# Kernel optimization log

Measured on AMD Instinct MI355X. Metric: run time of the kernel, lower is better.

Reference implementation:

```python
import jax, jax.numpy as jnp
import numpy as np

B, S, D = 2, 2048, 1024
H, DH = 16, 64  # num_heads, hidden_dimension (per-head)


def setup_inputs() -> dict:
    key = jax.random.key(0)
    ks = jax.random.split(key, 9)
    s = 1.0 / np.sqrt(D)
    so = 1.0 / np.sqrt(H * DH)
    return {
        "x": jax.random.normal(ks[0], (B, S, D), dtype=jnp.float32),
        "Wq": jax.random.uniform(ks[1], (D, H * DH), jnp.float32, -s, s),
        "bq": jax.random.uniform(ks[2], (H * DH,), jnp.float32, -s, s),
        "Wk": jax.random.uniform(ks[3], (D, H * DH), jnp.float32, -s, s),
        "bk": jax.random.uniform(ks[4], (H * DH,), jnp.float32, -s, s),
        "Wv": jax.random.uniform(ks[5], (D, H * DH), jnp.float32, -s, s),
        "bv": jax.random.uniform(ks[6], (H * DH,), jnp.float32, -s, s),
        "Wo": jax.random.uniform(ks[7], (H * DH, D), jnp.float32, -so, so),
        "bo": jax.random.uniform(ks[8], (D,), jnp.float32, -so, so),
    }


def reference(x, Wq, bq, Wk, bk, Wv, bv, Wo, bo):
    b, s, _ = x.shape
    # project and split heads: [b, h, s, dh]
    q = (x @ Wq + bq).reshape(b, s, H, DH).transpose(0, 2, 1, 3)
    k = (x @ Wk + bk).reshape(b, s, H, DH).transpose(0, 2, 1, 3)
    v = (x @ Wv + bv).reshape(b, s, H, DH).transpose(0, 2, 1, 3)
    scores = jnp.einsum('bhqd,bhkd->bhqk', q, k) / jnp.sqrt(jnp.float32(DH))
    causal = jnp.triu(jnp.ones((s, s), dtype=bool), k=1)
    scores = jnp.where(causal, -jnp.inf, scores)
    weights = jax.nn.softmax(scores, axis=-1)
    out = jnp.einsum('bhqk,bhkd->bhqd', weights, v)
    out = out.transpose(0, 2, 1, 3).reshape(b, s, H * DH)
    return out @ Wo + bo
```

## Files before the change

kernel.cpp:

```cpp
#include <hip/hip_runtime.h>

#define B_  2
#define S_  2048
#define D_  1024
#define H_  16
#define DH_ 64
#define NDH (H_*DH_)
#define BS_ (B_*S_)
#define PER ((size_t)B_*H_*S_*DH_)

typedef __bf16 bf16;
typedef bf16 bf16x8 __attribute__((ext_vector_type(8)));
typedef bf16 bf16x4 __attribute__((ext_vector_type(4)));
typedef float f32x4 __attribute__((ext_vector_type(4)));

#define QSCALE 0.18033688011112042f

#define AS1 __attribute__((address_space(1)))
#define AS3 __attribute__((address_space(3)))
__device__ inline void gld16(const bf16* g, bf16* l) {
    __builtin_amdgcn_global_load_lds((const AS1 void*)g, (AS3 void*)l, 16, 0, 0);
}

__global__ __launch_bounds__(256) void prep(
        const float* __restrict__ x,
        const float* __restrict__ W0, const float* __restrict__ W1,
        const float* __restrict__ W2, const float* __restrict__ W3,
        bf16* __restrict__ xb, bf16* __restrict__ T0, bf16* __restrict__ T1,
        bf16* __restrict__ T2, bf16* __restrict__ T3) {
    __shared__ float T[32][33];
    int bid = blockIdx.x, t = threadIdx.x;
    if (bid < 4096) {
        int i = (bid * 256 + t) * 4;
        float4 v = *(const float4*)(x + i);
        bf16x4 o = { (bf16)v.x, (bf16)v.y, (bf16)v.z, (bf16)v.w };
        *(bf16x4*)(xb + i) = o;
        return;
    }
    int r2 = bid - 4096;
    int z = r2 >> 10, w = r2 & 1023;
    const float* W = (z == 0) ? W0 : (z == 1) ? W1 : (z == 2) ? W2 : W3;
    bf16* Wt = (z == 0) ? T0 : (z == 1) ? T1 : (z == 2) ? T2 : T3;
    int k0 = (w >> 5) * 32, n0 = (w & 31) * 32;
    int r = t >> 3, c = (t & 7) * 4;
    float4 v = *(const float4*)(W + (size_t)(k0 + r) * 1024 + n0 + c);
    T[c + 0][r] = v.x; T[c + 1][r] = v.y; T[c + 2][r] = v.z; T[c + 3][r] = v.w;
    __syncthreads();
    bf16x4 o = { (bf16)T[r][c], (bf16)T[r][c + 1], (bf16)T[r][c + 2], (bf16)T[r][c + 3] };
    *(bf16x4*)(Wt + (size_t)(n0 + r) * 1024 + k0 + c) = o;
}

__global__ __launch_bounds__(256) void qkv_gemm(
        const bf16* __restrict__ A, const bf16* __restrict__ Bt,
        const float* __restrict__ bq, const float* __restrict__ bk,
        const float* __restrict__ bv, bf16* __restrict__ Qout, bf16* __restrict__ Vt) {
    __shared__ __align__(16) bf16 As[2][128 * 32];
    __shared__ __align__(16) bf16 Bs[2][128 * 32];
    int tid = threadIdx.x, wave = tid >> 6, lane = tid & 63;
    int quad = lane >> 4, l16 = lane & 15;

    int flat = blockIdx.y * 24 + blockIdx.x;
    int swz  = (flat & 7) * 96 + (flat >> 3);
    int bm = (swz / 24) * 128, bn = (swz % 24) * 128;
    int wm = (wave >> 1) * 64, wn = (wave & 1) * 64;

    int sr = lane >> 2, sc = (lane & 3) * 8;
    const bf16* Ag0 = A + (size_t)(bm + (wave * 2 + 0) * 16 + sr) * 1024 + sc;
    const bf16* Ag1 = A + (size_t)(bm + (wave * 2 + 1) * 16 + sr) * 1024 + sc;
    const bf16* Bg0 = Bt + (size_t)(bn + (wave * 2 + 0) * 16 + sr) * 1024 + sc;
    const bf16* Bg1 = Bt + (size_t)(bn + (wave * 2 + 1) * 16 + sr) * 1024 + sc;
    int la0 = (wave * 2 + 0) * 512;
    int la1 = (wave * 2 + 1) * 512;

    f32x4 acc[4][4] = {};

    gld16(Ag0, &As[0][la0]);
    gld16(Ag1, &As[0][la1]);
    gld16(Bg0, &Bs[0][la0]);
    gld16(Bg1, &Bs[0][la1]);
    asm volatile("s_waitcnt vmcnt(0)" ::: "memory");
    __builtin_amdgcn_s_barrier();

    for (int t = 0; t < 32; ++t) {
        int cur = t & 1, nxt = cur ^ 1;
        if (t < 31) {
            int k0 = (t + 1) * 32;
            gld16(Ag0 + k0, &As[nxt][la0]);
            gld16(Ag1 + k0, &As[nxt][la1]);
            gld16(Bg0 + k0, &Bs[nxt][la0]);
            gld16(Bg1 + k0, &Bs[nxt][la1]);
        }
        bf16x8 af[4], bfr[4];
        #pragma unroll
        for (int i = 0; i < 4; ++i)
            af[i] = *(const bf16x8*)&As[cur][(wm + i * 16 + l16) * 32 + quad * 8];
        #pragma unroll
        for (int j = 0; j < 4; ++j)
            bfr[j] = *(const bf16x8*)&Bs[cur][(wn + j * 16 + l16) * 32 + quad * 8];
        #pragma unroll
        for (int i = 0; i < 4; ++i)
          #pragma unroll
          for (int j = 0; j < 4; ++j)
            acc[i][j] = __builtin_amdgcn_mfma_f32_16x16x32_bf16(af[i], bfr[j], acc[i][j], 0, 0, 0);
        asm volatile("s_waitcnt vmcnt(0)" ::: "memory");
        __builtin_amdgcn_s_barrier();
    }

    #pragma unroll
    for (int i = 0; i < 4; ++i)
      #pragma unroll
      for (int j = 0; j < 4; ++j) {
        int col = bn + wn + j * 16 + l16;
        float bias = (col < 1024) ? bq[col] : (col < 2048) ? bk[col - 1024] : bv[col - 2048];
        int qkv = col >> 10, cw = col & 1023;
        int hh = cw >> 6, d = cw & 63;
        int row0 = bm + wm + i * 16 + quad * 4;
        int bb = row0 >> 11, s0 = row0 & 2047;
        if (qkv < 2) {
            float scl = (qkv == 0) ? QSCALE : 1.0f;
            #pragma unroll
            for (int r = 0; r < 4; ++r)
                Qout[(size_t)qkv * PER + (((size_t)bb * H_ + hh) * S_ + s0 + r) * DH_ + d] =
                    (bf16)((acc[i][j][r] + bias) * scl);
        } else {
            bf16x4 pack;
            #pragma unroll
            for (int r = 0; r < 4; ++r) pack[r] = (bf16)(acc[i][j][r] + bias);
            *(bf16x4*)&Vt[(((size_t)bb * H_ + hh) * DH_ + d) * S_ + s0] = pack;
        }
      }
}

__global__ __launch_bounds__(256) void gemm_proj(
        const bf16* __restrict__ A, const bf16* __restrict__ Bt,
        const float* __restrict__ bias, float* __restrict__ out) {
    __shared__ __align__(16) bf16 As[2][128 * 32];
    __shared__ __align__(16) bf16 Bs[2][64 * 32];
    int tid = threadIdx.x, wave = tid >> 6, lane = tid & 63;
    int quad = lane >> 4, l16 = lane & 15;

    int flat = blockIdx.y * 16 + blockIdx.x;
    int swz  = (flat & 7) * 64 + (flat >> 3);
    int bm = (swz / 16) * 128, bn = (swz % 16) * 64;
    int wm = (wave >> 1) * 64, wn = (wave & 1) * 32;

    int sr = lane >> 2, sc = (lane & 3) * 8;
    const bf16* Ag0 = A + (size_t)(bm + (wave * 2 + 0) * 16 + sr) * 1024 + sc;
    const bf16* Ag1 = A + (size_t)(bm + (wave * 2 + 1) * 16 + sr) * 1024 + sc;
    const bf16* Bg0 = Bt + (size_t)(bn + wave * 16 + sr) * 1024 + sc;
    int la0 = (wave * 2 + 0) * 512;
    int la1 = (wave * 2 + 1) * 512;
    int lb0 = wave * 512;

    f32x4 acc[4][2] = {};

    gld16(Ag0, &As[0][la0]);
    gld16(Ag1, &As[0][la1]);
    gld16(Bg0, &Bs[0][lb0]);
    asm volatile("s_waitcnt vmcnt(0)" ::: "memory");
    __builtin_amdgcn_s_barrier();

    for (int t = 0; t < 32; ++t) {
        int cur = t & 1, nxt = cur ^ 1;
        if (t < 31) {
            int k0 = (t + 1) * 32;
            gld16(Ag0 + k0, &As[nxt][la0]);
            gld16(Ag1 + k0, &As[nxt][la1]);
            gld16(Bg0 + k0, &Bs[nxt][lb0]);
        }
        bf16x8 af[4], bfr[2];
        #pragma unroll
        for (int i = 0; i < 4; ++i)
            af[i] = *(const bf16x8*)&As[cur][(wm + i * 16 + l16) * 32 + quad * 8];
        #pragma unroll
        for (int j = 0; j < 2; ++j)
            bfr[j] = *(const bf16x8*)&Bs[cur][(wn + j * 16 + l16) * 32 + quad * 8];
        #pragma unroll
        for (int i = 0; i < 4; ++i)
          #pragma unroll
          for (int j = 0; j < 2; ++j)
            acc[i][j] = __builtin_amdgcn_mfma_f32_16x16x32_bf16(af[i], bfr[j], acc[i][j], 0, 0, 0);
        asm volatile("s_waitcnt vmcnt(0)" ::: "memory");
        __builtin_amdgcn_s_barrier();
    }

    #pragma unroll
    for (int i = 0; i < 4; ++i)
      #pragma unroll
      for (int j = 0; j < 2; ++j) {
        int col = bn + wn + j * 16 + l16;
        float b = bias[col];
        #pragma unroll
        for (int r = 0; r < 4; ++r) {
            int row = bm + wm + i * 16 + quad * 4 + r;
            out[(size_t)row * 1024 + col] = acc[i][j][r] + b;
        }
      }
}

__global__ __launch_bounds__(256) void flash10(
        const bf16* __restrict__ Q, const bf16* __restrict__ K,
        const bf16* __restrict__ Vt, bf16* __restrict__ O) {
    int bh = blockIdx.x;
    int b = bh >> 4, h = bh & 15;
    int t = 31 - blockIdx.y;
    int q0 = t * 64;
    int nkt = t + 1;
    int tid = threadIdx.x;
    int wave = tid >> 6, lane = tid & 63;
    int quad = lane >> 4, l16 = lane & 15;
    int lm = l16 & 7;

    __shared__ __align__(16) bf16 Kl[2][64 * 64];
    __shared__ __align__(16) bf16 Vl[2][64 * 64];
    __shared__ bf16 P[4][16][72];

    const bf16* Qb = Q + (size_t)bh * S_ * DH_;
    const bf16* Kb = K + (size_t)bh * S_ * DH_;
    const bf16* Vb = Vt + (size_t)bh * DH_ * S_;

    bf16x8 qf[2];
    {
        const bf16* qp = Qb + (size_t)(q0 + wave * 16 + l16) * DH_ + quad * 8;
        qf[0] = *(const bf16x8*)(qp);
        qf[1] = *(const bf16x8*)(qp + 32);
    }

    bf16x8 ones;
    #pragma unroll
    for (int j = 0; j < 8; ++j) ones[j] = (l16 == 0) ? (bf16)1.0f : (bf16)0.0f;

    f32x4 oacc[4] = {};
    f32x4 lacc = {};

    int r8 = lane >> 3, c8 = lane & 7;
    int sco = ((c8 ^ r8) * 8);

    auto stage = [&](int buf, int kt) {
        int kv0 = kt * 64;
        #pragma unroll
        for (int g = 0; g < 2; ++g) {
            int row = wave * 16 + g * 8;
            gld16(Kb + (size_t)(kv0 + row + r8) * DH_ + sco, &Kl[buf][row * 64]);
            gld16(Vb + (size_t)(row + r8) * S_ + kv0 + sco,   &Vl[buf][row * 64]);
        }
    };

    stage(0, 0);
    __syncthreads();

    for (int kt = 0; kt < nkt; ++kt) {
        int buf = kt & 1;
        if (kt + 1 < nkt) stage(buf ^ 1, kt + 1);
        int kv0 = kt * 64;

        bf16x8 kf[4][2];
        #pragma unroll
        for (int ns = 0; ns < 4; ++ns) {
            int row = ns * 16 + l16;
            kf[ns][0] = *(const bf16x8*)&Kl[buf][row * 64 + ((quad)     ^ lm) * 8];
            kf[ns][1] = *(const bf16x8*)&Kl[buf][row * 64 + ((4 + quad) ^ lm) * 8];
        }

        f32x4 sacc[4] = {};
        #pragma unroll
        for (int ns = 0; ns < 4; ++ns) {
            sacc[ns] = __builtin_amdgcn_mfma_f32_16x16x32_bf16(qf[0], kf[ns][0], sacc[ns], 0, 0, 0);
            sacc[ns] = __builtin_amdgcn_mfma_f32_16x16x32_bf16(qf[1], kf[ns][1], sacc[ns], 0, 0, 0);
        }

        bool diag = (kt == nkt - 1);
        #pragma unroll
        for (int ns = 0; ns < 4; ++ns)
          #pragma unroll
          for (int r = 0; r < 4; ++r) {
              float p = __builtin_amdgcn_exp2f(sacc[ns][r]);
              if (diag) {
                  int kv = kv0 + ns * 16 + l16;
                  int qq = q0 + wave * 16 + quad * 4 + r;
                  if (kv > qq) p = 0.f;
              }
              P[wave][quad * 4 + r][ns * 16 + l16] = (bf16)p;
          }

        #pragma unroll
        for (int ks = 0; ks < 2; ++ks) {
            bf16x8 pf = *(const bf16x8*)&P[wave][l16][ks * 32 + quad * 8];
            lacc = __builtin_amdgcn_mfma_f32_16x16x32_bf16(pf, ones, lacc, 0, 0, 0);
            #pragma unroll
            for (int ds = 0; ds < 4; ++ds) {
                bf16x8 vf = *(const bf16x8*)&Vl[buf][(ds * 16 + l16) * 64 + ((ks * 4 + quad) ^ lm) * 8];
                oacc[ds] = __builtin_amdgcn_mfma_f32_16x16x32_bf16(pf, vf, oacc[ds], 0, 0, 0);
            }
        }

        __syncthreads();
    }

    float ls[4];
    #pragma unroll
    for (int r = 0; r < 4; ++r) ls[r] = __shfl(lacc[r], quad << 4);
    #pragma unroll
    for (int ds = 0; ds < 4; ++ds)
      #pragma unroll
      for (int r = 0; r < 4; ++r) {
          int qq = q0 + wave * 16 + quad * 4 + r;
          O[((size_t)b * S_ + qq) * NDH + h * DH_ + ds * 16 + l16] = (bf16)(oacc[ds][r] / ls[r]);
      }
}

extern "C" void kernel_launch(void* const* d_in, const int* in_sizes, int n_in,
                              void* d_out, int out_size, void* d_ws, size_t ws_size,
                              hipStream_t stream) {
    const float* x  = (const float*)d_in[0];
    const float* Wq = (const float*)d_in[1];
    const float* bq = (const float*)d_in[2];
    const float* Wk = (const float*)d_in[3];
    const float* bk = (const float*)d_in[4];
    const float* Wv = (const float*)d_in[5];
    const float* bv = (const float*)d_in[6];
    const float* Wo = (const float*)d_in[7];
    const float* bo = (const float*)d_in[8];
    float* out = (float*)d_out;

    bf16* ws = (bf16*)d_ws;
    const size_t M1 = (size_t)1024 * 1024;
    bf16* xb    = ws;
    bf16* WqkvT = ws + 4 * M1;
    bf16* WoT   = ws + 7 * M1;
    bf16* Qw    = ws + 8 * M1;
    bf16* Vtw   = ws + 16 * M1;
    bf16* Ow    = ws + 20 * M1;

    prep<<<8192, 256, 0, stream>>>(x, Wq, Wk, Wv, Wo,
                                   xb, WqkvT, WqkvT + M1, WqkvT + 2 * M1, WoT);

    qkv_gemm<<<dim3(3072 / 128, BS_ / 128), 256, 0, stream>>>(xb, WqkvT, bq, bk, bv, Qw, Vtw);

    flash10<<<dim3(B_ * H_, 32), 256, 0, stream>>>(Qw, Qw + PER, Vtw, Ow);

    gemm_proj<<<dim3(1024 / 64, BS_ / 128), 256, 0, stream>>>(Ow, WoT, bo, out);
}
```

Measured before the change: 189.2 us.

## Triple-buffer GEMM K-loop and XOR-swizzle LDS tiles to cut bank conflicts

Both the QKV and output-projection GEMMs move from a double-buffered to a triple-buffered LDS pipeline. Loads run two k-tiles ahead, a partial vmcnt wait lets one stage stay in flight, and there is one barrier per iteration instead of a full drain. The global-to-LDS column chunk is XOR-swizzled by row, and the fragment reads apply the matching swizzle, to reduce LDS bank conflicts on the 16-byte row reads. This costs 50% more shared memory per block, which may lower occupancy, and relies on hand-counted vmcnt values being correct.

```diff
diff --git a/kernel.cpp b/kernel.cpp
--- a/kernel.cpp
+++ b/kernel.cpp
@@ -54,8 +54,8 @@
         const bf16* __restrict__ A, const bf16* __restrict__ Bt,
         const float* __restrict__ bq, const float* __restrict__ bk,
         const float* __restrict__ bv, bf16* __restrict__ Qout, bf16* __restrict__ Vt) {
-    __shared__ __align__(16) bf16 As[2][128 * 32];
-    __shared__ __align__(16) bf16 Bs[2][128 * 32];
+    __shared__ __align__(16) bf16 As[3][128 * 32];
+    __shared__ __align__(16) bf16 Bs[3][128 * 32];
     int tid = threadIdx.x, wave = tid >> 6, lane = tid & 63;
     int quad = lane >> 4, l16 = lane & 15;
 
@@ -64,7 +64,8 @@
     int bm = (swz / 24) * 128, bn = (swz % 24) * 128;
     int wm = (wave >> 1) * 64, wn = (wave & 1) * 64;
 
-    int sr = lane >> 2, sc = (lane & 3) * 8;
+    int sr = lane >> 2;
+    int sc = (((lane & 3) ^ ((sr ^ (sr >> 2)) & 3)) * 8);
     const bf16* Ag0 = A + (size_t)(bm + (wave * 2 + 0) * 16 + sr) * 1024 + sc;
     const bf16* Ag1 = A + (size_t)(bm + (wave * 2 + 1) * 16 + sr) * 1024 + sc;
     const bf16* Bg0 = Bt + (size_t)(bn + (wave * 2 + 0) * 16 + sr) * 1024 + sc;
@@ -72,39 +73,43 @@
     int la0 = (wave * 2 + 0) * 512;
     int la1 = (wave * 2 + 1) * 512;
 
+    int cs0 = ((0 ^ ((l16 ^ (l16 >> 2)) & 3)) ^ quad) * 8;
+    int rsw = (l16 ^ (l16 >> 2)) & 3;
+
     f32x4 acc[4][4] = {};
 
-    gld16(Ag0, &As[0][la0]);
-    gld16(Ag1, &As[0][la1]);
-    gld16(Bg0, &Bs[0][la0]);
-    gld16(Bg1, &Bs[0][la1]);
-    asm volatile("s_waitcnt vmcnt(0)" ::: "memory");
-    __builtin_amdgcn_s_barrier();
+    auto stage = [&](int buf, int t) {
+        int k0 = t * 32;
+        gld16(Ag0 + k0, &As[buf][la0]);
+        gld16(Ag1 + k0, &As[buf][la1]);
+        gld16(Bg0 + k0, &Bs[buf][la0]);
+        gld16(Bg1 + k0, &Bs[buf][la1]);
+    };
+    (void)cs0;
+
+    stage(0, 0);
+    stage(1, 1);
 
     for (int t = 0; t < 32; ++t) {
-        int cur = t & 1, nxt = cur ^ 1;
-        if (t < 31) {
-            int k0 = (t + 1) * 32;
-            gld16(Ag0 + k0, &As[nxt][la0]);
-            gld16(Ag1 + k0, &As[nxt][la1]);
-            gld16(Bg0 + k0, &Bs[nxt][la0]);
-            gld16(Bg1 + k0, &Bs[nxt][la1]);
-        }
+        if (t < 30) asm volatile("s_waitcnt vmcnt(4)" ::: "memory");
+        else        asm volatile("s_waitcnt vmcnt(0)" ::: "memory");
+        __builtin_amdgcn_s_barrier();
+        if (t + 2 < 32) stage((t + 2) % 3, t + 2);
+        int cur = t % 3;
         bf16x8 af[4], bfr[4];
         #pragma unroll
         for (int i = 0; i < 4; ++i)
-            af[i] = *(const bf16x8*)&As[cur][(wm + i * 16 + l16) * 32 + quad * 8];
+            af[i] = *(const bf16x8*)&As[cur][(wm + i * 16 + l16) * 32 + ((0 ^ quad ^ rsw)) * 8];
         #pragma unroll
         for (int j = 0; j < 4; ++j)
-            bfr[j] = *(const bf16x8*)&Bs[cur][(wn + j * 16 + l16) * 32 + quad * 8];
+            bfr[j] = *(const bf16x8*)&Bs[cur][(wn + j * 16 + l16) * 32 + ((0 ^ quad ^ rsw)) * 8];
         #pragma unroll
         for (int i = 0; i < 4; ++i)
           #pragma unroll
           for (int j = 0; j < 4; ++j)
             acc[i][j] = __builtin_amdgcn_mfma_f32_16x16x32_bf16(af[i], bfr[j], acc[i][j], 0, 0, 0);
-        asm volatile("s_waitcnt vmcnt(0)" ::: "memory");
-        __builtin_amdgcn_s_barrier();
-    }
+    }
+    __builtin_amdgcn_s_barrier();
 
     #pragma unroll
     for (int i = 0; i < 4; ++i)
@@ -134,8 +139,8 @@
 __global__ __launch_bounds__(256) void gemm_proj(
         const bf16* __restrict__ A, const bf16* __restrict__ Bt,
         const float* __restrict__ bias, float* __restrict__ out) {
-    __shared__ __align__(16) bf16 As[2][128 * 32];
-    __shared__ __align__(16) bf16 Bs[2][64 * 32];
+    __shared__ __align__(16) bf16 As[3][128 * 32];
+    __shared__ __align__(16) bf16 Bs[3][64 * 32];
     int tid = threadIdx.x, wave = tid >> 6, lane = tid & 63;
     int quad = lane >> 4, l16 = lane & 15;
 
@@ -144,7 +149,8 @@
     int bm = (swz / 16) * 128, bn = (swz % 16) * 64;
     int wm = (wave >> 1) * 64, wn = (wave & 1) * 32;
 
-    int sr = lane >> 2, sc = (lane & 3) * 8;
+    int sr = lane >> 2;
+    int sc = (((lane & 3) ^ ((sr ^ (sr >> 2)) & 3)) * 8);
     const bf16* Ag0 = A + (size_t)(bm + (wave * 2 + 0) * 16 + sr) * 1024 + sc;
     const bf16* Ag1 = A + (size_t)(bm + (wave * 2 + 1) * 16 + sr) * 1024 + sc;
     const bf16* Bg0 = Bt + (size_t)(bn + wave * 16 + sr) * 1024 + sc;
@@ -152,37 +158,40 @@
     int la1 = (wave * 2 + 1) * 512;
     int lb0 = wave * 512;
 
+    int rsw = (l16 ^ (l16 >> 2)) & 3;
+
     f32x4 acc[4][2] = {};
 
-    gld16(Ag0, &As[0][la0]);
-    gld16(Ag1, &As[0][la1]);
-    gld16(Bg0, &Bs[0][lb0]);
-    asm volatile("s_waitcnt vmcnt(0)" ::: "memory");
-    __builtin_amdgcn_s_barrier();
+    auto stage = [&](int buf, int t) {
+        int k0 = t * 32;
+        gld16(Ag0 + k0, &As[buf][la0]);
+        gld16(Ag1 + k0, &As[buf][la1]);
+        gld16(Bg0 + k0, &Bs[buf][lb0]);
+    };
+
+    stage(0, 0);
+    stage(1, 1);
 
     for (int t = 0; t < 32; ++t) {
-        int cur = t & 1, nxt = cur ^ 1;
-        if (t < 31) {
-            int k0 = (t + 1) * 32;
-            gld16(Ag0 + k0, &As[nxt][la0]);
-            gld16(Ag1 + k0, &As[nxt][la1]);
-            gld16(Bg0 + k0, &Bs[nxt][lb0]);
-        }
+        if (t < 30) asm volatile("s_waitcnt vmcnt(3)" ::: "memory");
+        else        asm volatile("s_waitcnt vmcnt(0)" ::: "memory");
+        __builtin_amdgcn_s_barrier();
+        if (t + 2 < 32) stage((t + 2) % 3, t + 2);
+        int cur = t % 3;
         bf16x8 af[4], bfr[2];
         #pragma unroll
         for (int i = 0; i < 4; ++i)
-            af[i] = *(const bf16x8*)&As[cur][(wm + i * 16 + l16) * 32 + quad * 8];
+            af[i] = *(const bf16x8*)&As[cur][(wm + i * 16 + l16) * 32 + (quad ^ rsw) * 8];
         #pragma unroll
         for (int j = 0; j < 2; ++j)
-            bfr[j] = *(const bf16x8*)&Bs[cur][(wn + j * 16 + l16) * 32 + quad * 8];
+            bfr[j] = *(const bf16x8*)&Bs[cur][(wn + j * 16 + l16) * 32 + (quad ^ rsw) * 8];
         #pragma unroll
         for (int i = 0; i < 4; ++i)
           #pragma unroll
           for (int j = 0; j < 2; ++j)
             acc[i][j] = __builtin_amdgcn_mfma_f32_16x16x32_bf16(af[i], bfr[j], acc[i][j], 0, 0, 0);
-        asm volatile("s_waitcnt vmcnt(0)" ::: "memory");
-        __builtin_amdgcn_s_barrier();
-    }
+    }
+    __builtin_amdgcn_s_barrier();
 
     #pragma unroll
     for (int i = 0; i < 4; ++i)
```

After: 182.7 us. 1.04x faster.
